# Kernel tuning notes

Measured on AMD Instinct MI355X. Metric: run time of the kernel, lower is better.

Reference implementation:

```python
import jax, jax.numpy as jnp
import numpy as np

LOG2E = 1.4426950408889634  # 1/ln(2): kernel works in log2 space with exp2


def _mlstm_chunkwise_single(q, k, v, vecI, vecF, chunk_size):
    # q,k: [T,K]; v: [T,V]; vecI,vecF: [T] (log2-space gate preactivations)
    T, K = q.shape
    V = v.shape[-1]
    BT = chunk_size
    NT = T // BT
    scale = K ** -0.5
    dt = q.dtype

    qc = q.reshape(NT, BT, K)
    kc = k.reshape(NT, BT, K)
    vc = v.reshape(NT, BT, V)
    ic = vecI.reshape(NT, BT)
    fc = vecF.reshape(NT, BT)
    b = jnp.cumsum(fc, axis=1)            # within-chunk cumulative log2 forget (vecF in kernel)
    f_last = b[:, -1]                      # scaF_last
    g = ic + f_last[:, None] - b           # decay from each pos to chunk end (vecG)

    tri = jnp.tril(jnp.ones((BT, BT), dtype=bool))

    def step(carry, inp):
        C, n, m = carry                    # [K,V], [K], scalar running max
        qt, kt, vt, it, bt, gt, fl = inp
        # intra-chunk decay matrix D[t,s] = i[s] + b[t] - b[s] for s<=t
        D = it[None, :] + bt[:, None] - bt[None, :]
        D = jnp.where(tri, D, -jnp.inf)
        m_intra = jnp.max(D, axis=1)                      # [BT]
        m_total = jnp.maximum(bt + m, m_intra)            # matM_total
        S = (qt @ kt.T) * (scale * jnp.exp2(D - m_total[:, None]))
        q_sc = qt * (scale * jnp.exp2(bt + m - m_total))[:, None]
        h_num = q_sc @ C + S @ vt                          # [BT,V]
        denom = jnp.maximum(jnp.abs(q_sc @ n + S.sum(axis=1)), jnp.exp2(-m_total))
        h = h_num / denom[:, None]
        # cross-chunk matrix-state recurrence with log2 restabilization
        m_next = jnp.maximum(fl + m, jnp.max(gt))
        dec = jnp.exp2(fl + m - m_next)
        kdec = kt * jnp.exp2(gt - m_next)[:, None]         # [BT,K]
        C_next = C * dec + kdec.T @ vt
        n_next = n * dec + kdec.sum(axis=0)
        return (C_next, n_next, m_next), h

    C0 = jnp.zeros((K, V), dt)
    n0 = jnp.zeros((K,), dt)
    m0 = jnp.zeros((), dt)
    _, hs = jax.lax.scan(step, (C0, n0, m0), (qc, kc, vc, ic, b, g, f_last))
    return hs.reshape(T, V)


def setup_inputs() -> dict:
    key = jax.random.key(0)
    ks = jax.random.split(key, 5)
    B, H, T, D = 8, 8, 4096, 64
    q = jax.random.normal(ks[0], (B, H, T, D), dtype=jnp.float32)
    k = jax.random.normal(ks[1], (B, H, T, D), dtype=jnp.float32)
    v = jax.random.normal(ks[2], (B, H, T, D), dtype=jnp.float32)
    i = jax.random.normal(ks[3], (B, H, T), dtype=jnp.float32)
    f = jax.random.normal(ks[4], (B, H, T), dtype=jnp.float32)
    return {"q": q, "k": k, "v": v, "i": i, "f": f, "chunk_size": 64}


def reference(q, k, v, i, f, chunk_size):
    B, H, T, K = q.shape
    V = v.shape[-1]
    vecF = jax.nn.log_sigmoid(f) * LOG2E   # log2 sigmoid(f)
    vecI = i * LOG2E                       # input gate in log2 space
    BH = B * H
    fn = lambda qq, kk, vv, ii, ff: _mlstm_chunkwise_single(qq, kk, vv, ii, ff, chunk_size)
    h = jax.vmap(fn)(q.reshape(BH, T, K), k.reshape(BH, T, K), v.reshape(BH, T, V),
                     vecI.reshape(BH, T), vecF.reshape(BH, T))
    return h.reshape(B, H, T, V)
```

## Files before the change

### kernel.cpp

```cpp
#include <hip/hip_runtime.h>
#include <hip/hip_bf16.h>
#include <math.h>

#define LOG2E_F 1.4426950408889634f

static constexpr int BT = 64;
static constexpr int DK = 64;
static constexpr int DV = 64;
static constexpr float SCALE = 0.125f;
static constexpr int PAD = 72;

typedef unsigned short ushort_t;
typedef __attribute__((ext_vector_type(8))) short short8;
typedef __attribute__((ext_vector_type(4))) float f32x4;
typedef __attribute__((ext_vector_type(4))) ushort_t ushort4v;

#define MFMA16(a, b, c) __builtin_amdgcn_mfma_f32_16x16x32_bf16((a), (b), (c), 0, 0, 0)

__device__ __forceinline__ float logsig_log2e(float x){
    float l = (x >= 0.f) ? (-log1pf(expf(-x))) : (x - log1pf(expf(x)));
    return l * LOG2E_F;
}
__device__ __forceinline__ ushort_t f2bf(float x){
    unsigned u = __builtin_bit_cast(unsigned, x);
    unsigned r = u + 0x7FFFu + ((u >> 16) & 1u);
    return (ushort_t)(r >> 16);
}
__device__ __forceinline__ float bf2f(ushort_t u){
    return __builtin_bit_cast(float, ((unsigned)u) << 16);
}
__device__ __forceinline__ void split_bf(float x, ushort_t& h, ushort_t& l){
    h = f2bf(x);
    l = f2bf(x - bf2f(h));
}

__global__ __launch_bounds__(256) void stageA_kernel(
    const float* __restrict__ kg, const float* __restrict__ vg,
    const float* __restrict__ ig, const float* __restrict__ fg,
    float* __restrict__ A_ws, float* __restrict__ nloc_ws,
    float* __restrict__ fl_ws, float* __restrict__ mloc_ws,
    int T, int NT)
{
    const int ct = blockIdx.x, s = blockIdx.y, tid = threadIdx.x;
    const int w = tid >> 6, lane = tid & 63, ln = lane & 15, quad = lane >> 4;
    const int q8 = quad * 8;

    __shared__ __align__(16) ushort_t kth[DK][PAD];
    __shared__ __align__(16) ushort_t ktl[DK][PAD];
    __shared__ __align__(16) ushort_t vth[DV][PAD];
    __shared__ __align__(16) ushort_t vtl[DV][PAD];
    __shared__ float gsc[BT];

    const size_t rowbase = (size_t)s * T + (size_t)ct * BT;
    const float* kc = kg + rowbase * DK;
    const float* vc = vg + rowbase * DV;

    float4 kr[4], vr[4];
    #pragma unroll
    for (int i = 0; i < 4; ++i){
        int idx = i * 1024 + tid * 4;
        kr[i] = *(const float4*)(kc + idx);
        vr[i] = *(const float4*)(vc + idx);
    }
    if (tid < 64){
        float b = logsig_log2e(fg[rowbase + tid]);
        #pragma unroll
        for (int off = 1; off < 64; off <<= 1){
            float y = __shfl_up(b, off);
            if (tid >= off) b += y;
        }
        float f_last = __shfl(b, 63);
        float a = ig[rowbase + tid] * LOG2E_F - b;
        float p = a;
        #pragma unroll
        for (int off = 32; off > 0; off >>= 1) p = fmaxf(p, __shfl_xor(p, off));
        gsc[tid] = exp2f(a - p);
        if (tid == 0){ fl_ws[s * NT + ct] = f_last; mloc_ws[s * NT + ct] = f_last + p; }
    }
    __syncthreads();
    #pragma unroll
    for (int i = 0; i < 4; ++i){
        int idx = i * 1024 + tid * 4;
        int r = idx >> 6, c0 = idx & 63;
        float g = gsc[r];
        float kv[4] = {kr[i].x * g, kr[i].y * g, kr[i].z * g, kr[i].w * g};
        float vv[4] = {vr[i].x, vr[i].y, vr[i].z, vr[i].w};
        #pragma unroll
        for (int j = 0; j < 4; ++j){
            ushort_t h, l;
            split_bf(kv[j], h, l); kth[c0 + j][r] = h; ktl[c0 + j][r] = l;
            split_bf(vv[j], h, l); vth[c0 + j][r] = h; vtl[c0 + j][r] = l;
        }
    }
    __syncthreads();

    const int m = 16 * w + ln;
    short8 ah0 = *(const short8*)&kth[m][q8];
    short8 ah1 = *(const short8*)&kth[m][32 + q8];
    short8 al0 = *(const short8*)&ktl[m][q8];
    short8 al1 = *(const short8*)&ktl[m][32 + q8];
    float* Ab = A_ws + (size_t)(s * NT + ct) * 4096;
    #pragma unroll
    for (int t = 0; t < 4; ++t){
        f32x4 acc = {0.f, 0.f, 0.f, 0.f};
        short8 bh0 = *(const short8*)&vth[16 * t + ln][q8];
        short8 bh1 = *(const short8*)&vth[16 * t + ln][32 + q8];
        short8 bl0 = *(const short8*)&vtl[16 * t + ln][q8];
        short8 bl1 = *(const short8*)&vtl[16 * t + ln][32 + q8];
        acc = MFMA16(ah0, bh0, acc);
        acc = MFMA16(ah1, bh1, acc);
        acc = MFMA16(ah0, bl0, acc);
        acc = MFMA16(ah1, bl1, acc);
        acc = MFMA16(al0, bh0, acc);
        acc = MFMA16(al1, bh1, acc);
        #pragma unroll
        for (int reg = 0; reg < 4; ++reg){
            int row = 16 * w + quad * 4 + reg;
            Ab[t * 1024 + row * 16 + ln] = acc[reg];
        }
    }
    if (tid < 64){
        float a = 0.f;
        #pragma unroll
        for (int c = 0; c < BT; ++c) a += bf2f(kth[tid][c]) + bf2f(ktl[tid][c]);
        nloc_ws[((size_t)(s * NT + ct)) * DK + tid] = a;
    }
}

__global__ __launch_bounds__(256) void stageB_kernel(
    const float* __restrict__ A_ws, const float* __restrict__ nloc_ws,
    const float* __restrict__ fl_ws, const float* __restrict__ mloc_ws,
    float* __restrict__ Cws, float* __restrict__ nws, float* __restrict__ mws,
    int NT)
{
    const int vb = blockIdx.x, s = blockIdx.y, tid = threadIdx.x;
    __shared__ float decs[64], scs[64];

    if (tid < 64){
        float fl = fl_ws[s * NT + tid];
        float ml = mloc_ws[s * NT + tid];
        float F = fl, G = ml;
        #pragma unroll
        for (int off = 1; off < 64; off <<= 1){
            float Fp = __shfl_up(F, off);
            float Gp = __shfl_up(G, off);
            if (tid >= off){ G = fmaxf(Gp + F, G); F = Fp + F; }
        }
        float m_next = fmaxf(F, G);
        float m_cur  = __shfl_up(m_next, 1);
        if (tid == 0) m_cur = 0.f;
        decs[tid] = exp2f(fl + m_cur - m_next);
        scs[tid]  = exp2f(ml - m_next);
        if (vb == 0) mws[s * NT + tid] = m_cur;
    }
    __syncthreads();

    const size_t base = (size_t)s * NT * 4096 + (size_t)vb * 1024 + tid * 4;
    const float* Ab = A_ws + base;
    float*       Cb = Cws  + base;
    const bool do_n = (vb == 0) && (tid < 64);

    float4 C4 = make_float4(0.f, 0.f, 0.f, 0.f);
    float nreg = 0.f;
    float4 p[8]; float nl[8];
    #pragma unroll
    for (int i = 0; i < 8; ++i){
        p[i] = *(const float4*)(Ab + (size_t)i * 4096);
        nl[i] = 0.f;
    }
    if (do_n){
        #pragma unroll
        for (int i = 0; i < 8; ++i) nl[i] = nloc_ws[((size_t)(s * NT + i)) * DK + tid];
    }
    const float4 z4 = make_float4(0.f, 0.f, 0.f, 0.f);

    for (int t0 = 0; t0 < NT; t0 += 8){
        float4 q[8]; float nq[8];
        const int tn = t0 + 8;
        #pragma unroll
        for (int i = 0; i < 8; ++i)
            q[i] = (tn + i < NT) ? *(const float4*)(Ab + (size_t)(tn + i) * 4096) : z4;
        #pragma unroll
        for (int i = 0; i < 8; ++i) nq[i] = 0.f;
        if (do_n){
            #pragma unroll
            for (int i = 0; i < 8; ++i)
                if (tn + i < NT) nq[i] = nloc_ws[((size_t)(s * NT + tn + i)) * DK + tid];
        }
        #pragma unroll
        for (int i = 0; i < 8; ++i){
            const int t = t0 + i;
            *(float4*)(Cb + (size_t)t * 4096) = C4;
            if (do_n) nws[((size_t)(s * NT + t)) * DK + tid] = nreg;
            const float d = decs[t], sc = scs[t];
            C4.x = C4.x * d + p[i].x * sc;
            C4.y = C4.y * d + p[i].y * sc;
            C4.z = C4.z * d + p[i].z * sc;
            C4.w = C4.w * d + p[i].w * sc;
            if (do_n) nreg = nreg * d + nl[i] * sc;
        }
        #pragma unroll
        for (int i = 0; i < 8; ++i){ p[i] = q[i]; nl[i] = nq[i]; }
    }
}

__global__ __launch_bounds__(256) void pass2_kernel(
    const float* __restrict__ qg, const float* __restrict__ kg, const float* __restrict__ vg,
    const float* __restrict__ ig, const float* __restrict__ fg,
    const float* __restrict__ Cws, const float* __restrict__ nws, const float* __restrict__ mws,
    float* __restrict__ out, int T, int NT)
{
    const int ct = blockIdx.x, s = blockIdx.y, tid = threadIdx.x;
    const int w = tid >> 6, lane = tid & 63, ln = lane & 15, quad = lane >> 4;
    const int q8 = quad * 8;

    __shared__ __align__(16) ushort_t q_hi[BT][PAD];
    __shared__ __align__(16) ushort_t q_lo[BT][PAD];
    __shared__ __align__(16) ushort_t kC_hi[BT][PAD];
    __shared__ __align__(16) ushort_t kC_lo[BT][PAD];
    __shared__ __align__(16) ushort_t vt_hi[DV][PAD];
    __shared__ __align__(16) ushort_t Z_bf[BT][PAD];
    __shared__ float colterm[BT], Mr[BT], rowfac[BT], dncl[BT];
    __shared__ float nsh[DK], qn[BT], rowsum[BT];

    const size_t rowbase = (size_t)s * T + (size_t)ct * BT;
    const float* qc = qg + rowbase * DK;
    const float* kc = kg + rowbase * DK;
    const float* vc = vg + rowbase * DV;
    const float* Cc = Cws + ((size_t)(s * NT + ct)) * 4096;
    const float* nc = nws + ((size_t)(s * NT + ct)) * DK;
    const float m   = mws[s * NT + ct];

    float4 qr[4], kr4[4], vr[4], Cr[4];
    #pragma unroll
    for (int i = 0; i < 4; ++i){
        int idx = i * 1024 + tid * 4;
        qr[i]  = *(const float4*)(qc + idx);
        kr4[i] = *(const float4*)(kc + idx);
        vr[i]  = *(const float4*)(vc + idx);
        Cr[i]  = *(const float4*)(Cc + idx);
    }
    if (tid < 64){
        float b = logsig_log2e(fg[rowbase + tid]);
        #pragma unroll
        for (int off = 1; off < 64; off <<= 1){
            float y = __shfl_up(b, off);
            if (tid >= off) b += y;
        }
        float a = ig[rowbase + tid] * LOG2E_F - b;
        float p = a;
        #pragma unroll
        for (int off = 1; off < 64; off <<= 1){
            float y = __shfl_up(p, off);
            if (tid >= off) p = fmaxf(p, y);
        }
        float M = fmaxf(m, p);
        colterm[tid] = a;
        Mr[tid] = M;
        rowfac[tid] = SCALE * exp2f(m - M);
        dncl[tid] = exp2f(-(b + M));
        nsh[tid] = nc[tid];
    }
    #pragma unroll
    for (int i = 0; i < 4; ++i){
        int idx = i * 1024 + tid * 4;
        int r = idx >> 6, c0 = idx & 63;
        float qv[4] = {qr[i].x, qr[i].y, qr[i].z, qr[i].w};
        float kv[4] = {kr4[i].x, kr4[i].y, kr4[i].z, kr4[i].w};
        float vv[4] = {vr[i].x, vr[i].y, vr[i].z, vr[i].w};
        ushort4v qh4, ql4, kh4, kl4;
        #pragma unroll
        for (int j = 0; j < 4; ++j){
            ushort_t h, l;
            split_bf(qv[j], h, l); qh4[j] = h; ql4[j] = l;
            split_bf(kv[j], h, l); kh4[j] = h; kl4[j] = l;
            vt_hi[c0 + j][r] = f2bf(vv[j]);
        }
        *(ushort4v*)&q_hi[r][c0] = qh4;
        *(ushort4v*)&q_lo[r][c0] = ql4;
        *(ushort4v*)&kC_hi[r][c0] = kh4;
        *(ushort4v*)&kC_lo[r][c0] = kl4;
    }
    __syncthreads();

    const int mrow = 16 * w + ln;
    short8 ah0 = *(const short8*)&q_hi[mrow][q8];
    short8 ah1 = *(const short8*)&q_hi[mrow][32 + q8];
    short8 al0 = *(const short8*)&q_lo[mrow][q8];
    short8 al1 = *(const short8*)&q_lo[mrow][32 + q8];

    {
        float p = 0.f;
        #pragma unroll
        for (int j = 0; j < 8; ++j){
            float qv0 = bf2f((ushort_t)ah0[j]) + bf2f((ushort_t)al0[j]);
            float qv1 = bf2f((ushort_t)ah1[j]) + bf2f((ushort_t)al1[j]);
            p = fmaf(qv0, nsh[q8 + j], p);
            p = fmaf(qv1, nsh[32 + q8 + j], p);
        }
        p += __shfl_xor(p, 16);
        p += __shfl_xor(p, 32);
        if (quad == 0) qn[mrow] = p;
    }

    f32x4 sacc[4];
    #pragma unroll
    for (int t = 0; t < 4; ++t){
        sacc[t] = (f32x4){0.f, 0.f, 0.f, 0.f};
        short8 bh0 = *(const short8*)&kC_hi[16 * t + ln][q8];
        short8 bh1 = *(const short8*)&kC_hi[16 * t + ln][32 + q8];
        short8 bl0 = *(const short8*)&kC_lo[16 * t + ln][q8];
        short8 bl1 = *(const short8*)&kC_lo[16 * t + ln][32 + q8];
        sacc[t] = MFMA16(ah0, bh0, sacc[t]);
        sacc[t] = MFMA16(ah1, bh1, sacc[t]);
        sacc[t] = MFMA16(ah0, bl0, sacc[t]);
        sacc[t] = MFMA16(ah1, bl1, sacc[t]);
        sacc[t] = MFMA16(al0, bh0, sacc[t]);
        sacc[t] = MFMA16(al1, bh1, sacc[t]);
    }
    {
        float rsum[4] = {0.f, 0.f, 0.f, 0.f};
        float Mrv[4];
        #pragma unroll
        for (int reg = 0; reg < 4; ++reg) Mrv[reg] = Mr[16 * w + quad * 4 + reg];
        #pragma unroll
        for (int t = 0; t < 4; ++t){
            int c = 16 * t + ln;
            float cterm = colterm[c];
            #pragma unroll
            for (int reg = 0; reg < 4; ++reg){
                int r = 16 * w + quad * 4 + reg;
                float vS = (c <= r) ? sacc[t][reg] * SCALE * exp2f(cterm - Mrv[reg]) : 0.f;
                Z_bf[r][c] = f2bf(vS);
                rsum[reg] += vS;
            }
        }
        #pragma unroll
        for (int off = 1; off < 16; off <<= 1){
            #pragma unroll
            for (int reg = 0; reg < 4; ++reg) rsum[reg] += __shfl_xor(rsum[reg], off);
        }
        if (ln == 0){
            #pragma unroll
            for (int reg = 0; reg < 4; ++reg) rowsum[16 * w + quad * 4 + reg] = rsum[reg];
        }
    }
    __syncthreads();

    #pragma unroll
    for (int i = 0; i < 4; ++i){
        int idx = i * 1024 + tid * 4;
        int vsl = idx >> 10, krow = (idx >> 4) & 63, ci = idx & 15;
        int v0 = vsl * 16 + ci;
        float cv[4] = {Cr[i].x, Cr[i].y, Cr[i].z, Cr[i].w};
        #pragma unroll
        for (int j = 0; j < 4; ++j){
            ushort_t h, l;
            split_bf(cv[j], h, l);
            kC_hi[v0 + j][krow] = h;
            kC_lo[v0 + j][krow] = l;
        }
    }
    __syncthreads();

    f32x4 acc[4];
    #pragma unroll
    for (int t = 0; t < 4; ++t){
        acc[t] = (f32x4){0.f, 0.f, 0.f, 0.f};
        short8 bh0 = *(const short8*)&kC_hi[16 * t + ln][q8];
        short8 bh1 = *(const short8*)&kC_hi[16 * t + ln][32 + q8];
        short8 bl0 = *(const short8*)&kC_lo[16 * t + ln][q8];
        short8 bl1 = *(const short8*)&kC_lo[16 * t + ln][32 + q8];
        acc[t] = MFMA16(ah0, bh0, acc[t]);
        acc[t] = MFMA16(ah1, bh1, acc[t]);
        acc[t] = MFMA16(ah0, bl0, acc[t]);
        acc[t] = MFMA16(ah1, bl1, acc[t]);
        acc[t] = MFMA16(al0, bh0, acc[t]);
        acc[t] = MFMA16(al1, bh1, acc[t]);
    }
    float rf[4], inv[4];
    #pragma unroll
    for (int reg = 0; reg < 4; ++reg){
        int r = 16 * w + quad * 4 + reg;
        rf[reg] = rowfac[r];
        float dn = fabsf(rf[reg] * qn[r] + rowsum[r]);
        inv[reg] = 1.f / fmaxf(dn, dncl[r]);
    }
    #pragma unroll
    for (int t = 0; t < 4; ++t){
        #pragma unroll
        for (int reg = 0; reg < 4; ++reg) acc[t][reg] *= rf[reg];
    }
    short8 az0 = *(const short8*)&Z_bf[mrow][q8];
    short8 az1 = *(const short8*)&Z_bf[mrow][32 + q8];
    #pragma unroll
    for (int t = 0; t < 4; ++t){
        short8 bh0 = *(const short8*)&vt_hi[16 * t + ln][q8];
        short8 bh1 = *(const short8*)&vt_hi[16 * t + ln][32 + q8];
        acc[t] = MFMA16(az0, bh0, acc[t]);
        acc[t] = MFMA16(az1, bh1, acc[t]);
    }
    #pragma unroll
    for (int t = 0; t < 4; ++t){
        int c = 16 * t + ln;
        #pragma unroll
        for (int reg = 0; reg < 4; ++reg){
            int r = 16 * w + quad * 4 + reg;
            out[(rowbase + r) * DV + c] = acc[t][reg] * inv[reg];
        }
    }
}

__global__ __launch_bounds__(256) void fused_kernel(
    const float* __restrict__ qg, const float* __restrict__ kg, const float* __restrict__ vg,
    const float* __restrict__ ig, const float* __restrict__ fg,
    float* __restrict__ out, int T, int NT)
{
    const int s = blockIdx.x;
    const int tid = threadIdx.x;
    const int lane = tid & 63;

    __shared__ float X[BT][DK + 1];
    __shared__ float Y[BT][DK + 1];
    __shared__ float Cb[DK][DV];
    __shared__ __hip_bfloat16 Zh[BT][BT];
    __shared__ float colterm[BT], Mr[BT], rowfac[BT], dncl[BT], gscale[BT];
    __shared__ float nsh[DK], qn[BT], rowsum[BT], denom[BT];
    __shared__ float sh_dec;

    const float* qseq = qg + (size_t)s * T * DK;
    const float* kseq = kg + (size_t)s * T * DK;
    const float* vseq = vg + (size_t)s * T * DV;
    const float* iseq = ig + (size_t)s * T;
    const float* fseq = fg + (size_t)s * T;

    for (int idx = tid; idx < DK * DV; idx += 256) Cb[idx >> 6][idx & 63] = 0.f;
    if (tid < 64) nsh[lane] = 0.f;
    float m = 0.f;
    __syncthreads();

    const int r0 = (tid >> 4) * 4;
    const int c0 = (tid & 15) * 4;
    const int v0 = c0;

    for (int t = 0; t < NT; ++t){
        const size_t rb = (size_t)t * BT;
        if (tid < 64){
            float b = logsig_log2e(fseq[rb + lane]);
            #pragma unroll
            for (int off = 1; off < 64; off <<= 1){
                float y = __shfl_up(b, off);
                if (lane >= off) b += y;
            }
            float f_last = __shfl(b, 63);
            float a = iseq[rb + lane] * LOG2E_F - b;
            float p = a;
            #pragma unroll
            for (int off = 1; off < 64; off <<= 1){
                float y = __shfl_up(p, off);
                if (lane >= off) p = fmaxf(p, y);
            }
            float M = fmaxf(m, p);
            colterm[lane] = a;
            Mr[lane] = M;
            rowfac[lane] = SCALE * exp2f(m - M);
            dncl[lane] = exp2f(-(b + M));
            float g = a + f_last;
            float gm = g;
            #pragma unroll
            for (int off = 32; off > 0; off >>= 1) gm = fmaxf(gm, __shfl_xor(gm, off));
            float m_next = fmaxf(f_last + m, gm);
            gscale[lane] = exp2f(g - m_next);
            if (tid == 0) sh_dec = exp2f(f_last + m - m_next);
            m = m_next;
        }
        #pragma unroll
        for (int base = 0; base < BT * DK; base += 1024){
            int idx = base + tid * 4;
            int r = idx >> 6, c = idx & 63;
            float4 a4 = *(const float4*)(qseq + rb * DK + idx);
            X[r][c] = a4.x; X[r][c+1] = a4.y; X[r][c+2] = a4.z; X[r][c+3] = a4.w;
            float4 b4 = *(const float4*)(kseq + rb * DK + idx);
            Y[r][c] = b4.x; Y[r][c+1] = b4.y; Y[r][c+2] = b4.z; Y[r][c+3] = b4.w;
        }
        __syncthreads();

        float sacc[4][4] = {};
        for (int x = 0; x < DK; ++x){
            float xr[4], yc[4];
            #pragma unroll
            for (int j = 0; j < 4; ++j) xr[j] = X[r0 + j][x];
            #pragma unroll
            for (int j = 0; j < 4; ++j) yc[j] = Y[c0 + j][x];
            #pragma unroll
            for (int j = 0; j < 4; ++j)
                #pragma unroll
                for (int jj = 0; jj < 4; ++jj)
                    sacc[j][jj] = fmaf(xr[j], yc[jj], sacc[j][jj]);
        }
        float rs[4];
        #pragma unroll
        for (int j = 0; j < 4; ++j){
            int r = r0 + j;
            float Mrv = Mr[r];
            float acc = 0.f;
            #pragma unroll
            for (int jj = 0; jj < 4; ++jj){
                int c = c0 + jj;
                float vS = (c <= r) ? sacc[j][jj] * SCALE * exp2f(colterm[c] - Mrv) : 0.f;
                Zh[r][c] = __float2bfloat16(vS);
                acc += vS;
            }
            rs[j] = acc;
        }
        #pragma unroll
        for (int off = 1; off < 16; off <<= 1){
            #pragma unroll
            for (int j = 0; j < 4; ++j) rs[j] += __shfl_xor(rs[j], off);
        }
        if ((tid & 15) == 0){
            #pragma unroll
            for (int j = 0; j < 4; ++j) rowsum[r0 + j] = rs[j];
        }
        float acc1[4][4] = {};
        for (int x = 0; x < DK; ++x){
            float xr[4], yv[4];
            #pragma unroll
            for (int j = 0; j < 4; ++j) xr[j] = X[r0 + j][x];
            #pragma unroll
            for (int j = 0; j < 4; ++j) yv[j] = Cb[x][v0 + j];
            #pragma unroll
            for (int j = 0; j < 4; ++j)
                #pragma unroll
                for (int jj = 0; jj < 4; ++jj)
                    acc1[j][jj] = fmaf(xr[j], yv[jj], acc1[j][jj]);
        }
        if (tid < 64){
            float acc = 0.f;
            for (int x = 0; x < DK; ++x) acc = fmaf(X[lane][x], nsh[x], acc);
            qn[lane] = acc;
        }
        __syncthreads();

        #pragma unroll
        for (int base = 0; base < BT * DV; base += 1024){
            int idx = base + tid * 4;
            int r = idx >> 6, c = idx & 63;
            float4 a4 = *(const float4*)(vseq + rb * DV + idx);
            X[r][c] = a4.x; X[r][c+1] = a4.y; X[r][c+2] = a4.z; X[r][c+3] = a4.w;
        }
        if (tid < 64){
            float dn = fabsf(rowfac[lane] * qn[lane] + rowsum[lane]);
            denom[lane] = fmaxf(dn, dncl[lane]);
        }
        __syncthreads();

        float acc2[4][4] = {};
        for (int c = 0; c < BT; ++c){
            float zr[4], xv[4];
            #pragma unroll
            for (int j = 0; j < 4; ++j) zr[j] = __bfloat162float(Zh[r0 + j][c]);
            #pragma unroll
            for (int j = 0; j < 4; ++j) xv[j] = X[c][v0 + j];
            #pragma unroll
            for (int j = 0; j < 4; ++j)
                #pragma unroll
                for (int jj = 0; jj < 4; ++jj)
                    acc2[j][jj] = fmaf(zr[j], xv[jj], acc2[j][jj]);
        }
        #pragma unroll
        for (int j = 0; j < 4; ++j){
            int r = r0 + j;
            float rf = rowfac[r];
            float inv = 1.f / denom[r];
            float4 h4;
            h4.x = (acc1[j][0] * rf + acc2[j][0]) * inv;
            h4.y = (acc1[j][1] * rf + acc2[j][1]) * inv;
            h4.z = (acc1[j][2] * rf + acc2[j][2]) * inv;
            h4.w = (acc1[j][3] * rf + acc2[j][3]) * inv;
            *(float4*)(out + ((size_t)s * T + rb + r) * DV + v0) = h4;
        }
        {
            float dec = sh_dec;
            float cr[4][4];
            #pragma unroll
            for (int j = 0; j < 4; ++j)
                #pragma unroll
                for (int jj = 0; jj < 4; ++jj)
                    cr[j][jj] = Cb[r0 + j][c0 + jj] * dec;
            for (int c = 0; c < BT; ++c){
                float gs = gscale[c];
                float kd[4], xv[4];
                #pragma unroll
                for (int j = 0; j < 4; ++j) kd[j] = Y[c][r0 + j] * gs;
                #pragma unroll
                for (int jj = 0; jj < 4; ++jj) xv[jj] = X[c][c0 + jj];
                #pragma unroll
                for (int j = 0; j < 4; ++j)
                    #pragma unroll
                    for (int jj = 0; jj < 4; ++jj)
                        cr[j][jj] = fmaf(kd[j], xv[jj], cr[j][jj]);
            }
            #pragma unroll
            for (int j = 0; j < 4; ++j)
                #pragma unroll
                for (int jj = 0; jj < 4; ++jj)
                    Cb[r0 + j][c0 + jj] = cr[j][jj];
        }
        if (tid < 64){
            float acc = 0.f;
            for (int c = 0; c < BT; ++c) acc = fmaf(Y[c][lane], gscale[c], acc);
            nsh[lane] = nsh[lane] * sh_dec + acc;
        }
        __syncthreads();
    }
}

extern "C" void kernel_launch(void* const* d_in, const int* in_sizes, int n_in,
                              void* d_out, int out_size, void* d_ws, size_t ws_size,
                              hipStream_t stream)
{
    const float* q  = (const float*)d_in[0];
    const float* k  = (const float*)d_in[1];
    const float* v  = (const float*)d_in[2];
    const float* ii = (const float*)d_in[3];
    const float* ff = (const float*)d_in[4];
    float* out = (float*)d_out;

    const int T  = 4096;
    const int BH = in_sizes[3] / T;
    const int NT = T / BT;

    const size_t szC  = (size_t)BH * NT * DK * DV * sizeof(float);
    const size_t szA  = szC;
    const size_t szn  = (size_t)BH * NT * DK * sizeof(float);
    const size_t szs  = (size_t)BH * NT * sizeof(float);

    const size_t need_new = szA + szC + 2 * szn + 3 * szs;

    if (ws_size >= need_new){
        char* p = (char*)d_ws;
        float* A_ws    = (float*)p;            p += szA;
        float* Cws     = (float*)p;            p += szC;
        float* nloc_ws = (float*)p;            p += szn;
        float* nws     = (float*)p;            p += szn;
        float* fl_ws   = (float*)p;            p += szs;
        float* mloc_ws = (float*)p;            p += szs;
        float* mws     = (float*)p;
        stageA_kernel<<<dim3(NT, BH), 256, 0, stream>>>(k, v, ii, ff, A_ws, nloc_ws, fl_ws, mloc_ws, T, NT);
        stageB_kernel<<<dim3(4, BH), 256, 0, stream>>>(A_ws, nloc_ws, fl_ws, mloc_ws, Cws, nws, mws, NT);
        pass2_kernel<<<dim3(NT, BH), 256, 0, stream>>>(q, k, v, ii, ff, Cws, nws, mws, out, T, NT);
    } else {
        fused_kernel<<<dim3(BH), 256, 0, stream>>>(q, k, v, ii, ff, out, T, NT);
    }
}
```

Before: 311.2 us.

## Swizzle LDS layouts, shrink pass2 LDS, MFMA key sums, widen stageB grid

Measured after the change: 292.4 us. -6.0%, faster.

```diff
diff --git a/kernel.cpp b/kernel.cpp
--- a/kernel.cpp
+++ b/kernel.cpp
@@ -17,6 +17,10 @@
 
 #define MFMA16(a, b, c) __builtin_amdgcn_mfma_f32_16x16x32_bf16((a), (b), (c), 0, 0, 0)
 
+__device__ __forceinline__ int SWZ(int a, int b){ return a * PAD + (b ^ (((a >> 3) & 3) << 3)); }
+__device__ __forceinline__ int ZSW(int r, int c){ return r * PAD + (c ^ (((r >> 2) & 3) << 3)); }
+__device__ __forceinline__ int LIN(int r, int c){ return r * PAD + c; }
+
 __device__ __forceinline__ float logsig_log2e(float x){
     float l = (x >= 0.f) ? (-log1pf(expf(-x))) : (x - log1pf(expf(x)));
     return l * LOG2E_F;
@@ -34,7 +38,7 @@
     l = f2bf(x - bf2f(h));
 }
 
-__global__ __launch_bounds__(256) void stageA_kernel(
+__global__ __launch_bounds__(256, 4) void stageA_kernel(
     const float* __restrict__ kg, const float* __restrict__ vg,
     const float* __restrict__ ig, const float* __restrict__ fg,
     float* __restrict__ A_ws, float* __restrict__ nloc_ws,
@@ -45,10 +49,10 @@
     const int w = tid >> 6, lane = tid & 63, ln = lane & 15, quad = lane >> 4;
     const int q8 = quad * 8;
 
-    __shared__ __align__(16) ushort_t kth[DK][PAD];
-    __shared__ __align__(16) ushort_t ktl[DK][PAD];
-    __shared__ __align__(16) ushort_t vth[DV][PAD];
-    __shared__ __align__(16) ushort_t vtl[DV][PAD];
+    __shared__ __align__(16) ushort_t kth[BT * PAD];
+    __shared__ __align__(16) ushort_t ktl[BT * PAD];
+    __shared__ __align__(16) ushort_t vth[BT * PAD];
+    __shared__ __align__(16) ushort_t vtl[BT * PAD];
     __shared__ float gsc[BT];
 
     const size_t rowbase = (size_t)s * T + (size_t)ct * BT;
@@ -88,25 +92,25 @@
         #pragma unroll
         for (int j = 0; j < 4; ++j){
             ushort_t h, l;
-            split_bf(kv[j], h, l); kth[c0 + j][r] = h; ktl[c0 + j][r] = l;
-            split_bf(vv[j], h, l); vth[c0 + j][r] = h; vtl[c0 + j][r] = l;
+            split_bf(kv[j], h, l); kth[SWZ(c0 + j, r)] = h; ktl[SWZ(c0 + j, r)] = l;
+            split_bf(vv[j], h, l); vth[SWZ(c0 + j, r)] = h; vtl[SWZ(c0 + j, r)] = l;
         }
     }
     __syncthreads();
 
     const int m = 16 * w + ln;
-    short8 ah0 = *(const short8*)&kth[m][q8];
-    short8 ah1 = *(const short8*)&kth[m][32 + q8];
-    short8 al0 = *(const short8*)&ktl[m][q8];
-    short8 al1 = *(const short8*)&ktl[m][32 + q8];
+    short8 ah0 = *(const short8*)&kth[SWZ(m, q8)];
+    short8 ah1 = *(const short8*)&kth[SWZ(m, 32 + q8)];
+    short8 al0 = *(const short8*)&ktl[SWZ(m, q8)];
+    short8 al1 = *(const short8*)&ktl[SWZ(m, 32 + q8)];
     float* Ab = A_ws + (size_t)(s * NT + ct) * 4096;
     #pragma unroll
     for (int t = 0; t < 4; ++t){
         f32x4 acc = {0.f, 0.f, 0.f, 0.f};
-        short8 bh0 = *(const short8*)&vth[16 * t + ln][q8];
-        short8 bh1 = *(const short8*)&vth[16 * t + ln][32 + q8];
-        short8 bl0 = *(const short8*)&vtl[16 * t + ln][q8];
-        short8 bl1 = *(const short8*)&vtl[16 * t + ln][32 + q8];
+        short8 bh0 = *(const short8*)&vth[SWZ(16 * t + ln, q8)];
+        short8 bh1 = *(const short8*)&vth[SWZ(16 * t + ln, 32 + q8)];
+        short8 bl0 = *(const short8*)&vtl[SWZ(16 * t + ln, q8)];
+        short8 bl1 = *(const short8*)&vtl[SWZ(16 * t + ln, 32 + q8)];
         acc = MFMA16(ah0, bh0, acc);
         acc = MFMA16(ah1, bh1, acc);
         acc = MFMA16(ah0, bl0, acc);
@@ -119,11 +123,20 @@
             Ab[t * 1024 + row * 16 + ln] = acc[reg];
         }
     }
-    if (tid < 64){
-        float a = 0.f;
-        #pragma unroll
-        for (int c = 0; c < BT; ++c) a += bf2f(kth[tid][c]) + bf2f(ktl[tid][c]);
-        nloc_ws[((size_t)(s * NT + ct)) * DK + tid] = a;
+    {
+        short8 ones;
+        #pragma unroll
+        for (int j = 0; j < 8; ++j) ones[j] = (short)0x3F80;
+        f32x4 nacc = {0.f, 0.f, 0.f, 0.f};
+        nacc = MFMA16(ah0, ones, nacc);
+        nacc = MFMA16(ah1, ones, nacc);
+        nacc = MFMA16(al0, ones, nacc);
+        nacc = MFMA16(al1, ones, nacc);
+        if (ln == 0){
+            #pragma unroll
+            for (int reg = 0; reg < 4; ++reg)
+                nloc_ws[((size_t)(s * NT + ct)) * DK + 16 * w + quad * 4 + reg] = nacc[reg];
+        }
     }
 }
 
@@ -155,31 +168,26 @@
     }
     __syncthreads();
 
-    const size_t base = (size_t)s * NT * 4096 + (size_t)vb * 1024 + tid * 4;
+    const size_t base = (size_t)s * NT * 4096 + (size_t)vb * 256 + tid;
     const float* Ab = A_ws + base;
     float*       Cb = Cws  + base;
     const bool do_n = (vb == 0) && (tid < 64);
 
-    float4 C4 = make_float4(0.f, 0.f, 0.f, 0.f);
-    float nreg = 0.f;
-    float4 p[8]; float nl[8];
-    #pragma unroll
-    for (int i = 0; i < 8; ++i){
-        p[i] = *(const float4*)(Ab + (size_t)i * 4096);
-        nl[i] = 0.f;
-    }
+    float C = 0.f, nreg = 0.f;
+    float p[8], nl[8];
+    #pragma unroll
+    for (int i = 0; i < 8; ++i){ p[i] = Ab[(size_t)i * 4096]; nl[i] = 0.f; }
     if (do_n){
         #pragma unroll
         for (int i = 0; i < 8; ++i) nl[i] = nloc_ws[((size_t)(s * NT + i)) * DK + tid];
     }
-    const float4 z4 = make_float4(0.f, 0.f, 0.f, 0.f);
 
     for (int t0 = 0; t0 < NT; t0 += 8){
-        float4 q[8]; float nq[8];
+        float qv[8], nq[8];
         const int tn = t0 + 8;
         #pragma unroll
         for (int i = 0; i < 8; ++i)
-            q[i] = (tn + i < NT) ? *(const float4*)(Ab + (size_t)(tn + i) * 4096) : z4;
+            qv[i] = (tn + i < NT) ? Ab[(size_t)(tn + i) * 4096] : 0.f;
         #pragma unroll
         for (int i = 0; i < 8; ++i) nq[i] = 0.f;
         if (do_n){
@@ -190,21 +198,18 @@
         #pragma unroll
         for (int i = 0; i < 8; ++i){
             const int t = t0 + i;
-            *(float4*)(Cb + (size_t)t * 4096) = C4;
+            Cb[(size_t)t * 4096] = C;
             if (do_n) nws[((size_t)(s * NT + t)) * DK + tid] = nreg;
             const float d = decs[t], sc = scs[t];
-            C4.x = C4.x * d + p[i].x * sc;
-            C4.y = C4.y * d + p[i].y * sc;
-            C4.z = C4.z * d + p[i].z * sc;
-            C4.w = C4.w * d + p[i].w * sc;
+            C = C * d + p[i] * sc;
             if (do_n) nreg = nreg * d + nl[i] * sc;
         }
         #pragma unroll
-        for (int i = 0; i < 8; ++i){ p[i] = q[i]; nl[i] = nq[i]; }
-    }
-}
-
-__global__ __launch_bounds__(256) void pass2_kernel(
+        for (int i = 0; i < 8; ++i){ p[i] = qv[i]; nl[i] = nq[i]; }
+    }
+}
+
+__global__ __launch_bounds__(256, 4) void pass2_kernel(
     const float* __restrict__ qg, const float* __restrict__ kg, const float* __restrict__ vg,
     const float* __restrict__ ig, const float* __restrict__ fg,
     const float* __restrict__ Cws, const float* __restrict__ nws, const float* __restrict__ mws,
@@ -214,12 +219,10 @@
     const int w = tid >> 6, lane = tid & 63, ln = lane & 15, quad = lane >> 4;
     const int q8 = quad * 8;
 
-    __shared__ __align__(16) ushort_t q_hi[BT][PAD];
-    __shared__ __align__(16) ushort_t q_lo[BT][PAD];
-    __shared__ __align__(16) ushort_t kC_hi[BT][PAD];
-    __shared__ __align__(16) ushort_t kC_lo[BT][PAD];
-    __shared__ __align__(16) ushort_t vt_hi[DV][PAD];
-    __shared__ __align__(16) ushort_t Z_bf[BT][PAD];
+    __shared__ __align__(16) ushort_t bufA[BT * PAD];
+    __shared__ __align__(16) ushort_t bufB[BT * PAD];
+    __shared__ __align__(16) ushort_t bufC[BT * PAD];
+    __shared__ __align__(16) ushort_t bufD[BT * PAD];
     __shared__ float colterm[BT], Mr[BT], rowfac[BT], dncl[BT];
     __shared__ float nsh[DK], qn[BT], rowsum[BT];
 
@@ -267,27 +270,25 @@
         int r = idx >> 6, c0 = idx & 63;
         float qv[4] = {qr[i].x, qr[i].y, qr[i].z, qr[i].w};
         float kv[4] = {kr4[i].x, kr4[i].y, kr4[i].z, kr4[i].w};
-        float vv[4] = {vr[i].x, vr[i].y, vr[i].z, vr[i].w};
         ushort4v qh4, ql4, kh4, kl4;
         #pragma unroll
         for (int j = 0; j < 4; ++j){
             ushort_t h, l;
             split_bf(qv[j], h, l); qh4[j] = h; ql4[j] = l;
             split_bf(kv[j], h, l); kh4[j] = h; kl4[j] = l;
-            vt_hi[c0 + j][r] = f2bf(vv[j]);
-        }
-        *(ushort4v*)&q_hi[r][c0] = qh4;
-        *(ushort4v*)&q_lo[r][c0] = ql4;
-        *(ushort4v*)&kC_hi[r][c0] = kh4;
-        *(ushort4v*)&kC_lo[r][c0] = kl4;
+        }
+        *(ushort4v*)&bufA[LIN(r, c0)] = qh4;
+        *(ushort4v*)&bufB[LIN(r, c0)] = ql4;
+        *(ushort4v*)&bufC[SWZ(r, c0)] = kh4;
+        *(ushort4v*)&bufD[SWZ(r, c0)] = kl4;
     }
     __syncthreads();
 
     const int mrow = 16 * w + ln;
-    short8 ah0 = *(const short8*)&q_hi[mrow][q8];
-    short8 ah1 = *(const short8*)&q_hi[mrow][32 + q8];
-    short8 al0 = *(const short8*)&q_lo[mrow][q8];
-    short8 al1 = *(const short8*)&q_lo[mrow][32 + q8];
+    short8 ah0 = *(const short8*)&bufA[LIN(mrow, q8)];
+    short8 ah1 = *(const short8*)&bufA[LIN(mrow, 32 + q8)];
+    short8 al0 = *(const short8*)&bufB[LIN(mrow, q8)];
+    short8 al1 = *(const short8*)&bufB[LIN(mrow, 32 + q8)];
 
     {
         float p = 0.f;
@@ -302,15 +303,25 @@
         p += __shfl_xor(p, 32);
         if (quad == 0) qn[mrow] = p;
     }
+    __syncthreads();
+
+    #pragma unroll
+    for (int i = 0; i < 4; ++i){
+        int idx = i * 1024 + tid * 4;
+        int r = idx >> 6, c0 = idx & 63;
+        float vv[4] = {vr[i].x, vr[i].y, vr[i].z, vr[i].w};
+        #pragma unroll
+        for (int j = 0; j < 4; ++j) bufB[SWZ(c0 + j, r)] = f2bf(vv[j]);
+    }
 
     f32x4 sacc[4];
     #pragma unroll
     for (int t = 0; t < 4; ++t){
         sacc[t] = (f32x4){0.f, 0.f, 0.f, 0.f};
-        short8 bh0 = *(const short8*)&kC_hi[16 * t + ln][q8];
-        short8 bh1 = *(const short8*)&kC_hi[16 * t + ln][32 + q8];
-        short8 bl0 = *(const short8*)&kC_lo[16 * t + ln][q8];
-        short8 bl1 = *(const short8*)&kC_lo[16 * t + ln][32 + q8];
+        short8 bh0 = *(const short8*)&bufC[SWZ(16 * t + ln, q8)];
+        short8 bh1 = *(const short8*)&bufC[SWZ(16 * t + ln, 32 + q8)];
+        short8 bl0 = *(const short8*)&bufD[SWZ(16 * t + ln, q8)];
+        short8 bl1 = *(const short8*)&bufD[SWZ(16 * t + ln, 32 + q8)];
         sacc[t] = MFMA16(ah0, bh0, sacc[t]);
         sacc[t] = MFMA16(ah1, bh1, sacc[t]);
         sacc[t] = MFMA16(ah0, bl0, sacc[t]);
@@ -331,7 +342,7 @@
             for (int reg = 0; reg < 4; ++reg){
                 int r = 16 * w + quad * 4 + reg;
                 float vS = (c <= r) ? sacc[t][reg] * SCALE * exp2f(cterm - Mrv[reg]) : 0.f;
-                Z_bf[r][c] = f2bf(vS);
+                bufA[ZSW(r, c)] = f2bf(vS);
                 rsum[reg] += vS;
             }
         }
@@ -357,8 +368,8 @@
         for (int j = 0; j < 4; ++j){
             ushort_t h, l;
             split_bf(cv[j], h, l);
-            kC_hi[v0 + j][krow] = h;
-            kC_lo[v0 + j][krow] = l;
+            bufC[SWZ(v0 + j, krow)] = h;
+            bufD[SWZ(v0 + j, krow)] = l;
         }
     }
     __syncthreads();
@@ -367,10 +378,10 @@
     #pragma unroll
     for (int t = 0; t < 4; ++t){
         acc[t] = (f32x4){0.f, 0.f, 0.f, 0.f};
-        short8 bh0 = *(const short8*)&kC_hi[16 * t + ln][q8];
-        short8 bh1 = *(const short8*)&kC_hi[16 * t + ln][32 + q8];
-        short8 bl0 = *(const short8*)&kC_lo[16 * t + ln][q8];
-        short8 bl1 = *(const short8*)&kC_lo[16 * t + ln][32 + q8];
+        short8 bh0 = *(const short8*)&bufC[SWZ(16 * t + ln, q8)];
+        short8 bh1 = *(const short8*)&bufC[SWZ(16 * t + ln, 32 + q8)];
+        short8 bl0 = *(const short8*)&bufD[SWZ(16 * t + ln, q8)];
+        short8 bl1 = *(const short8*)&bufD[SWZ(16 * t + ln, 32 + q8)];
         acc[t] = MFMA16(ah0, bh0, acc[t]);
         acc[t] = MFMA16(ah1, bh1, acc[t]);
         acc[t] = MFMA16(ah0, bl0, acc[t]);
@@ -391,12 +402,12 @@
         #pragma unroll
         for (int reg = 0; reg < 4; ++reg) acc[t][reg] *= rf[reg];
     }
-    short8 az0 = *(const short8*)&Z_bf[mrow][q8];
-    short8 az1 = *(const short8*)&Z_bf[mrow][32 + q8];
+    short8 az0 = *(const short8*)&bufA[ZSW(mrow, q8)];
+    short8 az1 = *(const short8*)&bufA[ZSW(mrow, 32 + q8)];
     #pragma unroll
     for (int t = 0; t < 4; ++t){
-        short8 bh0 = *(const short8*)&vt_hi[16 * t + ln][q8];
-        short8 bh1 = *(const short8*)&vt_hi[16 * t + ln][32 + q8];
+        short8 bh0 = *(const short8*)&bufB[SWZ(16 * t + ln, q8)];
+        short8 bh1 = *(const short8*)&bufB[SWZ(16 * t + ln, 32 + q8)];
         acc[t] = MFMA16(az0, bh0, acc[t]);
         acc[t] = MFMA16(az1, bh1, acc[t]);
     }
@@ -648,7 +659,7 @@
         float* mloc_ws = (float*)p;            p += szs;
         float* mws     = (float*)p;
         stageA_kernel<<<dim3(NT, BH), 256, 0, stream>>>(k, v, ii, ff, A_ws, nloc_ws, fl_ws, mloc_ws, T, NT);
-        stageB_kernel<<<dim3(4, BH), 256, 0, stream>>>(A_ws, nloc_ws, fl_ws, mloc_ws, Cws, nws, mws, NT);
+        stageB_kernel<<<dim3(16, BH), 256, 0, stream>>>(A_ws, nloc_ws, fl_ws, mloc_ws, Cws, nws, mws, NT);
         pass2_kernel<<<dim3(NT, BH), 256, 0, stream>>>(q, k, v, ii, ff, Cws, nws, mws, out, T, NT);
     } else {
         fused_kernel<<<dim3(BH), 256, 0, stream>>>(q, k, v, ii, ff, out, T, NT);
```
